# Kernel tuning notes

Hardware: AMD Instinct MI355X
Metric: run time of the kernel (lower is better)

## Reference

```python
import jax, jax.numpy as jnp
import numpy as np

D_MODEL = 1024
NUM_HEADS = 16
D_HEAD = D_MODEL // NUM_HEADS
WINDOW = 512
N_GLOBAL = 1


def longformer_mask(seq_len):
    # sliding window |i-j| <= window//2, plus global rows/cols for first N_GLOBAL tokens
    i = jnp.arange(seq_len)[:, None]
    j = jnp.arange(seq_len)[None, :]
    allowed = (jnp.abs(i - j) <= WINDOW // 2) | (i < N_GLOBAL) | (j < N_GLOBAL)
    return jnp.where(allowed, 0.0, -jnp.inf).astype(jnp.float32)


def setup_inputs() -> dict:
    key = jax.random.key(0)
    ks = jax.random.split(key, 6)
    B, S = 2, 2048
    scale = 1.0 / np.sqrt(D_MODEL)
    return {
        "hidden_states": jax.random.normal(ks[0], (B, S, D_MODEL), dtype=jnp.float32),
        "Wq": jax.random.normal(ks[1], (D_MODEL, D_MODEL), dtype=jnp.float32) * scale,
        "Wk": jax.random.normal(ks[2], (D_MODEL, D_MODEL), dtype=jnp.float32) * scale,
        "Wv": jax.random.normal(ks[3], (D_MODEL, D_MODEL), dtype=jnp.float32) * scale,
        "Wo": jax.random.normal(ks[4], (D_MODEL, D_MODEL), dtype=jnp.float32) * scale,
        "bo": jax.random.normal(ks[5], (D_MODEL,), dtype=jnp.float32) * 0.01,
    }


def reference(hidden_states, Wq, Wk, Wv, Wo, bo):
    B, S, _ = hidden_states.shape
    q = (hidden_states @ Wq).reshape(B, S, NUM_HEADS, D_HEAD).transpose(0, 2, 1, 3)
    k = (hidden_states @ Wk).reshape(B, S, NUM_HEADS, D_HEAD).transpose(0, 2, 1, 3)
    v = (hidden_states @ Wv).reshape(B, S, NUM_HEADS, D_HEAD).transpose(0, 2, 1, 3)
    mask = longformer_mask(S)  # [S, S]
    scores = jnp.einsum('bhqd,bhkd->bhqk', q, k) / np.sqrt(D_HEAD)
    scores = scores + mask[None, None]
    attn = jax.nn.softmax(scores, axis=-1)
    out = jnp.einsum('bhqk,bhkd->bhqd', attn, v)
    out = out.transpose(0, 2, 1, 3).reshape(B, S, D_MODEL)
    return out @ Wo + bo
```

## Files before the change

kernel.cpp:

```cpp
#include <hip/hip_runtime.h>
#include <cstdint>
#include <cstddef>

#define DM 1024
#define NH 16
#define DH 64
#define SEQ 2048
#define NB 2
#define WIN2 256
#define QBLK 64
#define KBLK 128

typedef float f32x4 __attribute__((ext_vector_type(4)));
typedef __bf16 bf16x8 __attribute__((ext_vector_type(8)));
typedef unsigned short u16x8 __attribute__((ext_vector_type(8)));
typedef unsigned short u16x4 __attribute__((ext_vector_type(4)));
typedef float f32x4v __attribute__((ext_vector_type(4)));

__device__ __forceinline__ unsigned short f2bf(float x) {
  unsigned int u = __float_as_uint(x);
  u += 0x7FFFu + ((u >> 16) & 1u);
  return (unsigned short)(u >> 16);
}
__device__ __forceinline__ float bf2f(unsigned short h) {
  return __uint_as_float(((unsigned int)h) << 16);
}
__device__ __forceinline__ f32x4 mfma_bf16(u16x8 a, u16x8 b, f32x4 c) {
  return __builtin_amdgcn_mfma_f32_16x16x32_bf16(
      __builtin_bit_cast(bf16x8, a), __builtin_bit_cast(bf16x8, b), c, 0, 0, 0);
}

__global__ __launch_bounds__(256) void hsplit_kernel(
    const float* __restrict__ x, unsigned short* __restrict__ hi,
    unsigned short* __restrict__ lo, int n4) {
  int i = blockIdx.x * 256 + threadIdx.x;
  int stride = gridDim.x * 256;
  for (; i < n4; i += stride) {
    f32x4v v = *(const f32x4v*)(x + (size_t)i * 4);
    u16x4 h, l;
#pragma unroll
    for (int j = 0; j < 4; ++j) {
      h[j] = f2bf(v[j]);
      l[j] = f2bf(v[j] - bf2f(h[j]));
    }
    *(u16x4*)(hi + (size_t)i * 4) = h;
    *(u16x4*)(lo + (size_t)i * 4) = l;
  }
}

__global__ __launch_bounds__(256) void wsplit_kernel(
    const float* __restrict__ W0, const float* __restrict__ W1,
    const float* __restrict__ W2, const float* __restrict__ W3,
    unsigned short* __restrict__ pwhi, unsigned short* __restrict__ pwlo) {
  __shared__ float tile[32][33];
  const float* W = blockIdx.z == 0 ? W0 : blockIdx.z == 1 ? W1 : blockIdx.z == 2 ? W2 : W3;
  unsigned short* ohi = pwhi + (size_t)blockIdx.z * DM * DM;
  unsigned short* olo = pwlo + (size_t)blockIdx.z * DM * DM;
  int k0 = blockIdx.y * 32, n0 = blockIdx.x * 32;
  int c = threadIdx.x & 31, r0 = threadIdx.x >> 5;
#pragma unroll
  for (int i = 0; i < 4; ++i) {
    int r = r0 + i * 8;
    tile[r][c] = W[(size_t)(k0 + r) * DM + n0 + c];
  }
  __syncthreads();
#pragma unroll
  for (int i = 0; i < 4; ++i) {
    int nr = r0 + i * 8;
    float v = tile[c][nr];
    unsigned short h = f2bf(v);
    unsigned short l = f2bf(v - bf2f(h));
    ohi[(size_t)(n0 + nr) * DM + k0 + c] = h;
    olo[(size_t)(n0 + nr) * DM + k0 + c] = l;
  }
}

template <int MODE>
__global__ __launch_bounds__(256) void gemm_split_kernel(
    const unsigned short* __restrict__ Ahi, const unsigned short* __restrict__ Alo,
    const unsigned short* __restrict__ Wthi, const unsigned short* __restrict__ Wtlo,
    unsigned short* __restrict__ Qo, unsigned short* __restrict__ Ko,
    unsigned short* __restrict__ Vo, float* __restrict__ Out,
    const float* __restrict__ bias) {
  __shared__ alignas(16) unsigned short sAh[128][40];
  __shared__ alignas(16) unsigned short sAl[128][40];
  __shared__ alignas(16) unsigned short sBh[128][40];
  __shared__ alignas(16) unsigned short sBl[128][40];
  const int t = threadIdx.x;
  const int lane = t & 63, wave = t >> 6;
  const int l15 = lane & 15, l4 = lane >> 4;
  const int wr = wave >> 1, wc = wave & 1;
  const int mB = blockIdx.y, nB = blockIdx.x, wz = blockIdx.z;
  const unsigned short* Bh = Wthi + (size_t)(MODE == 0 ? wz : 3) * DM * DM;
  const unsigned short* Bl = Wtlo + (size_t)(MODE == 0 ? wz : 3) * DM * DM;
  f32x4 acc[4][4];
#pragma unroll
  for (int m = 0; m < 4; ++m)
#pragma unroll
    for (int n = 0; n < 4; ++n) acc[m][n] = (f32x4)0.0f;

  for (int kt = 0; kt < DM / 32; ++kt) {
    __syncthreads();
#pragma unroll
    for (int i = 0; i < 2; ++i) {
      int slot = t + i * 256;
      int row = slot >> 2, c8 = slot & 3;
      size_t ga = (size_t)(mB * 128 + row) * DM + kt * 32 + c8 * 8;
      *(u16x8*)&sAh[row][c8 * 8] = *(const u16x8*)(Ahi + ga);
      *(u16x8*)&sAl[row][c8 * 8] = *(const u16x8*)(Alo + ga);
      size_t gb = (size_t)(nB * 128 + row) * DM + kt * 32 + c8 * 8;
      *(u16x8*)&sBh[row][c8 * 8] = *(const u16x8*)(Bh + gb);
      *(u16x8*)&sBl[row][c8 * 8] = *(const u16x8*)(Bl + gb);
    }
    __syncthreads();
    u16x8 ah[4], al[4];
#pragma unroll
    for (int m = 0; m < 4; ++m) {
      ah[m] = *(const u16x8*)&sAh[wr * 64 + m * 16 + l15][8 * l4];
      al[m] = *(const u16x8*)&sAl[wr * 64 + m * 16 + l15][8 * l4];
    }
#pragma unroll
    for (int n = 0; n < 4; ++n) {
      u16x8 bh = *(const u16x8*)&sBh[wc * 64 + n * 16 + l15][8 * l4];
      u16x8 bl = *(const u16x8*)&sBl[wc * 64 + n * 16 + l15][8 * l4];
#pragma unroll
      for (int m = 0; m < 4; ++m) {
        acc[m][n] = mfma_bf16(ah[m], bh, acc[m][n]);
        acc[m][n] = mfma_bf16(ah[m], bl, acc[m][n]);
        acc[m][n] = mfma_bf16(al[m], bh, acc[m][n]);
      }
    }
  }
#pragma unroll
  for (int m = 0; m < 4; ++m)
#pragma unroll
    for (int n = 0; n < 4; ++n)
#pragma unroll
      for (int r = 0; r < 4; ++r) {
        int rg = mB * 128 + wr * 64 + m * 16 + l4 * 4 + r;
        int cg = nB * 128 + wc * 64 + n * 16 + l15;
        float v = acc[m][n][r];
        if constexpr (MODE == 0) {
          int b = rg >> 11, s = rg & 2047, h = cg >> 6, d = cg & 63;
          size_t o = ((size_t)((b << 4) + h) * SEQ + s) * DH + d;
          unsigned short bf = f2bf(v);
          if (wz == 0) Qo[o] = bf;
          else if (wz == 1) Ko[o] = bf;
          else Vo[o] = bf;
        } else {
          Out[(size_t)rg * DM + cg] = v + bias[cg];
        }
      }
}

__global__ __launch_bounds__(256) void attn_kernel(
    const unsigned short* __restrict__ Qg, const unsigned short* __restrict__ Kg,
    const unsigned short* __restrict__ Vg, unsigned short* __restrict__ Ohi,
    unsigned short* __restrict__ Olo) {
  __shared__ alignas(16) unsigned short sQ[QBLK][72];
  __shared__ alignas(16) unsigned short sK[KBLK][72];
  __shared__ alignas(16) unsigned short sVt[DH][136];
  __shared__ alignas(16) unsigned short sP[QBLK][136];
  const int t = threadIdx.x;
  const int lane = t & 63, wave = t >> 6;
  const int l15 = lane & 15, l4 = lane >> 4;
  const int qb = blockIdx.x, h = blockIdx.y, b = blockIdx.z;
  const int q0 = qb * QBLK;
  const size_t hb = ((size_t)b * NH + h) * SEQ * DH;
  const int wrow = wave * 16;

#pragma unroll
  for (int i = 0; i < 2; ++i) {
    int slot = t + i * 256;
    int row = slot >> 3, c8 = slot & 7;
    *(u16x8*)&sQ[row][c8 * 8] =
        *(const u16x8*)(Qg + hb + (size_t)(q0 + row) * DH + c8 * 8);
  }

  f32x4 oacc[4];
#pragma unroll
  for (int n = 0; n < 4; ++n) oacc[n] = (f32x4)0.0f;
  float mrun[4], lrun[4];
#pragma unroll
  for (int r = 0; r < 4; ++r) { mrun[r] = -3.0e38f; lrun[r] = 0.0f; }

  const int tlo = (q0 >= WIN2) ? ((q0 - WIN2) >> 7) : 0;
  int thi = (q0 + QBLK - 1 + WIN2) >> 7;
  if (thi > SEQ / KBLK - 1) thi = SEQ / KBLK - 1;

  for (int tt = 0; tt < SEQ / KBLK; ++tt) {
    bool visit = (tt == 0) || (qb == 0) || (tt >= tlo && tt <= thi);
    if (!visit) continue;
    __syncthreads();
#pragma unroll
    for (int i = 0; i < 4; ++i) {
      int slot = t + i * 256;
      int row = slot >> 3, c8 = slot & 7;
      *(u16x8*)&sK[row][c8 * 8] =
          *(const u16x8*)(Kg + hb + (size_t)(tt * KBLK + row) * DH + c8 * 8);
    }
#pragma unroll
    for (int i = 0; i < 4; ++i) {
      int slot = t + i * 256;
      int row = slot >> 3, c8 = slot & 7;
      u16x8 v = *(const u16x8*)(Vg + hb + (size_t)(tt * KBLK + row) * DH + c8 * 8);
#pragma unroll
      for (int jj = 0; jj < 8; ++jj) sVt[c8 * 8 + jj][row] = v[jj];
    }
    __syncthreads();

    f32x4 sc[8];
#pragma unroll
    for (int n = 0; n < 8; ++n) sc[n] = (f32x4)0.0f;
#pragma unroll
    for (int ks = 0; ks < 2; ++ks) {
      u16x8 qa = *(const u16x8*)&sQ[wrow + l15][ks * 32 + 8 * l4];
#pragma unroll
      for (int n = 0; n < 8; ++n) {
        u16x8 kb = *(const u16x8*)&sK[n * 16 + l15][ks * 32 + 8 * l4];
        sc[n] = mfma_bf16(qa, kb, sc[n]);
      }
    }
    const int iabs_base = q0 + wrow + l4 * 4;
    float tmax[4];
#pragma unroll
    for (int r = 0; r < 4; ++r) tmax[r] = -3.0e38f;
#pragma unroll
    for (int n = 0; n < 8; ++n) {
      int jabs = tt * KBLK + n * 16 + l15;
#pragma unroll
      for (int r = 0; r < 4; ++r) {
        int iabs = iabs_base + r;
        float s = sc[n][r] * 0.125f;
        int dd = iabs - jabs; if (dd < 0) dd = -dd;
        bool ok = (dd <= WIN2) || (iabs < 1) || (jabs < 1);
        s = ok ? s : -1.0e30f;
        sc[n][r] = s;
        tmax[r] = fmaxf(tmax[r], s);
      }
    }
#pragma unroll
    for (int r = 0; r < 4; ++r) {
      float v = tmax[r];
      v = fmaxf(v, __shfl_xor(v, 1));
      v = fmaxf(v, __shfl_xor(v, 2));
      v = fmaxf(v, __shfl_xor(v, 4));
      v = fmaxf(v, __shfl_xor(v, 8));
      tmax[r] = v;
    }
    float scl[4], tsum[4];
#pragma unroll
    for (int r = 0; r < 4; ++r) {
      float mnew = fmaxf(mrun[r], tmax[r]);
      scl[r] = __expf(mrun[r] - mnew);
      mrun[r] = mnew;
      tsum[r] = 0.0f;
    }
#pragma unroll
    for (int n = 0; n < 8; ++n) {
#pragma unroll
      for (int r = 0; r < 4; ++r) {
        float p = __expf(sc[n][r] - mrun[r]);
        sc[n][r] = p;
        tsum[r] += p;
      }
    }
#pragma unroll
    for (int r = 0; r < 4; ++r) {
      float v = tsum[r];
      v += __shfl_xor(v, 1);
      v += __shfl_xor(v, 2);
      v += __shfl_xor(v, 4);
      v += __shfl_xor(v, 8);
      lrun[r] = lrun[r] * scl[r] + v;
    }
#pragma unroll
    for (int n = 0; n < 4; ++n)
#pragma unroll
      for (int r = 0; r < 4; ++r) oacc[n][r] *= scl[r];
#pragma unroll
    for (int n = 0; n < 8; ++n)
#pragma unroll
      for (int r = 0; r < 4; ++r)
        sP[wrow + l4 * 4 + r][n * 16 + l15] = f2bf(sc[n][r]);
    __syncthreads();
#pragma unroll
    for (int kt4 = 0; kt4 < 4; ++kt4) {
      u16x8 pa = *(const u16x8*)&sP[wrow + l15][kt4 * 32 + 8 * l4];
#pragma unroll
      for (int n = 0; n < 4; ++n) {
        u16x8 vb = *(const u16x8*)&sVt[n * 16 + l15][kt4 * 32 + 8 * l4];
        oacc[n] = mfma_bf16(pa, vb, oacc[n]);
      }
    }
  }
#pragma unroll
  for (int n = 0; n < 4; ++n)
#pragma unroll
    for (int r = 0; r < 4; ++r) {
      int srow = q0 + wrow + l4 * 4 + r;
      int d = n * 16 + l15;
      float v = oacc[n][r] / lrun[r];
      unsigned short uhi = f2bf(v);
      unsigned short ulo = f2bf(v - bf2f(uhi));
      size_t o = ((size_t)b * SEQ + srow) * DM + h * DH + d;
      Ohi[o] = uhi;
      Olo[o] = ulo;
    }
}

extern "C" void kernel_launch(void* const* d_in, const int* in_sizes, int n_in,
                              void* d_out, int out_size, void* d_ws, size_t ws_size,
                              hipStream_t stream) {
  const float* hid = (const float*)d_in[0];
  const float* Wq = (const float*)d_in[1];
  const float* Wk = (const float*)d_in[2];
  const float* Wv = (const float*)d_in[3];
  const float* Wo = (const float*)d_in[4];
  const float* bo = (const float*)d_in[5];
  float* out = (float*)d_out;

  const size_t HS = (size_t)NB * SEQ * DM;
  unsigned short* hhi = (unsigned short*)d_ws;
  unsigned short* hlo = hhi + HS;
  unsigned short* wthi = hlo + HS;
  unsigned short* wtlo = wthi + (size_t)4 * DM * DM;
  unsigned short* Qb = wtlo + (size_t)4 * DM * DM;
  unsigned short* Kb = Qb + HS;
  unsigned short* Vb = Kb + HS;
  unsigned short* attn_hi = hhi;
  unsigned short* attn_lo = hlo;

  hsplit_kernel<<<dim3(2048), dim3(256), 0, stream>>>(hid, hhi, hlo, (int)(HS / 4));
  wsplit_kernel<<<dim3(32, 32, 4), dim3(256), 0, stream>>>(Wq, Wk, Wv, Wo, wthi, wtlo);
  gemm_split_kernel<0><<<dim3(8, 32, 3), dim3(256), 0, stream>>>(
      hhi, hlo, wthi, wtlo, Qb, Kb, Vb, nullptr, nullptr);
  attn_kernel<<<dim3(SEQ / QBLK, NH, NB), dim3(256), 0, stream>>>(
      Qb, Kb, Vb, attn_hi, attn_lo);
  gemm_split_kernel<1><<<dim3(8, 32, 1), dim3(256), 0, stream>>>(
      attn_hi, attn_lo, wthi, wtlo, nullptr, nullptr, nullptr, out, bo);
}
```

Before: 396.2 us.

## Store V transposed from projection GEMM, keep Q in registers, drop P barrier

The QKV projection GEMM now writes V in a [b,h,d,s] transposed layout, so the attention kernel can fill its transposed V tile with vector loads instead of scattered 2-byte LDS writes. Q fragments are loaded straight into registers rather than staged through shared memory. The barrier between writing P and reading it is removed, since each wave reads only its own rows of sP. The GEMM epilogue's V stores become strided along the sequence axis, which may hurt coalescing there.

```diff
diff --git a/kernel.cpp b/kernel.cpp
--- a/kernel.cpp
+++ b/kernel.cpp
@@ -142,11 +142,14 @@
         float v = acc[m][n][r];
         if constexpr (MODE == 0) {
           int b = rg >> 11, s = rg & 2047, h = cg >> 6, d = cg & 63;
-          size_t o = ((size_t)((b << 4) + h) * SEQ + s) * DH + d;
           unsigned short bf = f2bf(v);
-          if (wz == 0) Qo[o] = bf;
-          else if (wz == 1) Ko[o] = bf;
-          else Vo[o] = bf;
+          if (wz == 0) {
+            Qo[((size_t)((b << 4) + h) * SEQ + s) * DH + d] = bf;
+          } else if (wz == 1) {
+            Ko[((size_t)((b << 4) + h) * SEQ + s) * DH + d] = bf;
+          } else {
+            Vo[((size_t)((b << 4) + h) * DH + d) * SEQ + s] = bf;
+          }
         } else {
           Out[(size_t)rg * DM + cg] = v + bias[cg];
         }
@@ -155,9 +158,8 @@
 
 __global__ __launch_bounds__(256) void attn_kernel(
     const unsigned short* __restrict__ Qg, const unsigned short* __restrict__ Kg,
-    const unsigned short* __restrict__ Vg, unsigned short* __restrict__ Ohi,
+    const unsigned short* __restrict__ Vtg, unsigned short* __restrict__ Ohi,
     unsigned short* __restrict__ Olo) {
-  __shared__ alignas(16) unsigned short sQ[QBLK][72];
   __shared__ alignas(16) unsigned short sK[KBLK][72];
   __shared__ alignas(16) unsigned short sVt[DH][136];
   __shared__ alignas(16) unsigned short sP[QBLK][136];
@@ -169,13 +171,10 @@
   const size_t hb = ((size_t)b * NH + h) * SEQ * DH;
   const int wrow = wave * 16;
 
-#pragma unroll
-  for (int i = 0; i < 2; ++i) {
-    int slot = t + i * 256;
-    int row = slot >> 3, c8 = slot & 7;
-    *(u16x8*)&sQ[row][c8 * 8] =
-        *(const u16x8*)(Qg + hb + (size_t)(q0 + row) * DH + c8 * 8);
-  }
+  u16x8 qreg[2];
+#pragma unroll
+  for (int ks = 0; ks < 2; ++ks)
+    qreg[ks] = *(const u16x8*)(Qg + hb + (size_t)(q0 + wrow + l15) * DH + ks * 32 + 8 * l4);
 
   f32x4 oacc[4];
 #pragma unroll
@@ -202,10 +201,9 @@
 #pragma unroll
     for (int i = 0; i < 4; ++i) {
       int slot = t + i * 256;
-      int row = slot >> 3, c8 = slot & 7;
-      u16x8 v = *(const u16x8*)(Vg + hb + (size_t)(tt * KBLK + row) * DH + c8 * 8);
-#pragma unroll
-      for (int jj = 0; jj < 8; ++jj) sVt[c8 * 8 + jj][row] = v[jj];
+      int d = slot >> 4, c16 = slot & 15;
+      *(u16x8*)&sVt[d][c16 * 8] =
+          *(const u16x8*)(Vtg + hb + (size_t)d * SEQ + tt * KBLK + c16 * 8);
     }
     __syncthreads();
 
@@ -214,11 +212,10 @@
     for (int n = 0; n < 8; ++n) sc[n] = (f32x4)0.0f;
 #pragma unroll
     for (int ks = 0; ks < 2; ++ks) {
-      u16x8 qa = *(const u16x8*)&sQ[wrow + l15][ks * 32 + 8 * l4];
 #pragma unroll
       for (int n = 0; n < 8; ++n) {
         u16x8 kb = *(const u16x8*)&sK[n * 16 + l15][ks * 32 + 8 * l4];
-        sc[n] = mfma_bf16(qa, kb, sc[n]);
+        sc[n] = mfma_bf16(qreg[ks], kb, sc[n]);
       }
     }
     const int iabs_base = q0 + wrow + l4 * 4;
@@ -283,7 +280,6 @@
 #pragma unroll
       for (int r = 0; r < 4; ++r)
         sP[wrow + l4 * 4 + r][n * 16 + l15] = f2bf(sc[n][r]);
-    __syncthreads();
 #pragma unroll
     for (int kt4 = 0; kt4 < 4; ++kt4) {
       u16x8 pa = *(const u16x8*)&sP[wrow + l15][kt4 * 32 + 8 * l4];
@@ -327,16 +323,16 @@
   unsigned short* wtlo = wthi + (size_t)4 * DM * DM;
   unsigned short* Qb = wtlo + (size_t)4 * DM * DM;
   unsigned short* Kb = Qb + HS;
-  unsigned short* Vb = Kb + HS;
+  unsigned short* Vtb = Kb + HS;
   unsigned short* attn_hi = hhi;
   unsigned short* attn_lo = hlo;
 
   hsplit_kernel<<<dim3(2048), dim3(256), 0, stream>>>(hid, hhi, hlo, (int)(HS / 4));
   wsplit_kernel<<<dim3(32, 32, 4), dim3(256), 0, stream>>>(Wq, Wk, Wv, Wo, wthi, wtlo);
   gemm_split_kernel<0><<<dim3(8, 32, 3), dim3(256), 0, stream>>>(
-      hhi, hlo, wthi, wtlo, Qb, Kb, Vb, nullptr, nullptr);
+      hhi, hlo, wthi, wtlo, Qb, Kb, Vtb, nullptr, nullptr);
   attn_kernel<<<dim3(SEQ / QBLK, NH, NB), dim3(256), 0, stream>>>(
-      Qb, Kb, Vb, attn_hi, attn_lo);
+      Qb, Kb, Vtb, attn_hi, attn_lo);
   gemm_split_kernel<1><<<dim3(8, 32, 1), dim3(256), 0, stream>>>(
       attn_hi, attn_lo, wthi, wtlo, nullptr, nullptr, nullptr, out, bo);
 }
```

New measurement: 340.4 us. 1.16x faster.
